# Kernel tuning notes

Hardware: AMD Instinct MI355X
Metric: run time of the kernel (lower is better)

## Reference

```python
import jax, jax.numpy as jnp
import numpy as np

B, F = 4096, 2048          # batch, inp_dim
H, D = 16, 128             # head_num, head_dim
NB, DB = 16, 8             # BlockLinear: head_dim split into head_num blocks of size head_dim//head_num
KER = 4
PROJ = int((4.0 / 3.0) * H * D)   # 2730
LN_EPS = float(F)          # flax quirk: nn.LayerNorm(inp_dim) sets epsilon positionally -> epsilon = 2048.0
GN_EPS = 1e-6              # flax GroupNorm default epsilon
EPS = 1e-8                 # module eps


def setup_inputs() -> dict:
    key = jax.random.key(0)
    ks = jax.random.split(key, 16)
    s = 0.02  # weight init scale for numerical sanity
    hd = H * D
    d = {}
    d['inputs'] = jax.random.normal(ks[0], (B, F), jnp.float32)
    d['c'] = jax.random.normal(ks[1], (B, hd), jnp.float32)
    d['n'] = jnp.ones((B, hd), jnp.float32)
    d['h'] = jax.random.normal(ks[2], (B, hd), jnp.float32)
    d['m'] = jnp.zeros((B, hd), jnp.float32)
    d['x_prev'] = jax.random.normal(ks[3], (B, KER - 1, F), jnp.float32)
    d['ln_scale'] = jnp.ones((F,), jnp.float32)
    d['ln_bias'] = jnp.zeros((F,), jnp.float32)
    for i, g in enumerate('zifo'):
        d['W' + g + '_k'] = jax.random.normal(ks[4 + i], (F, hd), jnp.float32) * s
        d['W' + g + '_b'] = jnp.zeros((hd,), jnp.float32)
        d['R' + g + '_k'] = jax.random.normal(ks[8 + i], (NB, DB, DB), jnp.float32) * s
        d['R' + g + '_b'] = jnp.zeros((NB, DB), jnp.float32)
    d['gn_scale'] = jnp.ones((D,), jnp.float32)
    d['gn_bias'] = jnp.zeros((D,), jnp.float32)
    d['up_k'] = jax.random.normal(ks[12], (hd, 2 * PROJ), jnp.float32) * s
    d['up_b'] = jnp.zeros((2 * PROJ,), jnp.float32)
    d['down_k'] = jax.random.normal(ks[13], (PROJ, F), jnp.float32) * s
    d['down_b'] = jnp.zeros((F,), jnp.float32)
    return d


def _layer_norm(x, scale, bias, eps):
    mu = x.mean(-1, keepdims=True)
    var = x.var(-1, keepdims=True)
    return (x - mu) / jnp.sqrt(var + eps) * scale + bias


def _group_norm(x, scale, bias, eps):
    # x: (B, H, D); flax GroupNorm(num_groups=H) groups the channel (last) dim,
    # reducing over all non-batch axes within each group.
    b, hh, dd = x.shape
    xg = x.reshape(b, hh, H, dd // H)
    mu = xg.mean(axis=(1, 3), keepdims=True)
    var = xg.var(axis=(1, 3), keepdims=True)
    xn = ((xg - mu) / jnp.sqrt(var + eps)).reshape(b, hh, dd)
    return xn * scale + bias


def reference(inputs, c, n, h, m, x_prev, ln_scale, ln_bias,
              Wz_k, Wz_b, Rz_k, Rz_b, Wi_k, Wi_b, Ri_k, Ri_b,
              Wf_k, Wf_b, Rf_k, Rf_b, Wo_k, Wo_b, Ro_k, Ro_b,
              gn_scale, gn_bias, up_k, up_b, down_k, down_b):
    x_t = _layer_norm(inputs, ln_scale, ln_bias, LN_EPS)
    x_window = jnp.concatenate([x_prev, x_t[:, None, :]], axis=1)  # (B, KER, F)
    x_prev_new = x_window[:, 1:, :]
    x_c = x_t  # use_conv == False

    h4 = h.reshape(B, H, NB, DB)  # per-head block-split hidden

    def gate(Wk, Wb, Rk, Rb):
        rec = jnp.einsum('bhnd,nde->bhne', h4, Rk) + Rb  # block-diagonal recurrence
        return x_c @ Wk + Wb + rec.reshape(B, H * D)

    i_raw = gate(Wi_k, Wi_b, Ri_k, Ri_b)
    f_raw = gate(Wf_k, Wf_b, Rf_k, Rf_b)
    z_raw = gate(Wz_k, Wz_b, Rz_k, Rz_b)
    o_raw = gate(Wo_k, Wo_b, Ro_k, Ro_b)

    logfplusm = m + jax.nn.log_sigmoid(f_raw)
    m_t = jnp.where(jnp.all(n == 0.0, axis=-1, keepdims=True), i_raw,
                    jnp.maximum(i_raw, logfplusm))
    o_t = jax.nn.sigmoid(o_raw)
    i_t = jnp.exp(i_raw - m_t)
    f_t = jnp.exp(logfplusm - m_t)
    z_t = jnp.tanh(z_raw)

    c_t = f_t * c + i_t * z_t
    n_t = f_t * n + i_t
    h_t = o_t * (c_t / (n_t + EPS))

    outn = _group_norm(h_t.reshape(B, H, D), gn_scale, gn_bias, GN_EPS).reshape(B, H * D)
    u = outn @ up_k + up_b
    o1, o2 = jnp.split(u, 2, axis=-1)
    out = (o1 * jax.nn.gelu(o2)) @ down_k + down_b + inputs
    return (out, c_t, n_t, h_t, m_t, x_prev_new)
```

## Files before the change

### kernel.cpp

```cpp
#include <hip/hip_runtime.h>
#include <hip/hip_bf16.h>
#include <cstdint>

#define BB 4096
#define FF 2048
#define HD 2048
#define PROJ_N 2730
#define UPN 5460
#define UPN_PAD 5504
#define DK_PAD 2752

typedef __attribute__((ext_vector_type(8))) short bf16x8;
typedef __attribute__((ext_vector_type(4))) float f32x4;

__device__ __forceinline__ unsigned short f2bf(float f) {
  union { float f; unsigned int u; } x; x.f = f;
  unsigned int r = x.u + 0x7fffu + ((x.u >> 16) & 1u);
  return (unsigned short)(r >> 16);
}

__global__ __launch_bounds__(256) void ln_prep(
    const float* __restrict__ inputs, const float* __restrict__ x_prev,
    const float* __restrict__ n_state,
    const float* __restrict__ ln_scale, const float* __restrict__ ln_bias,
    unsigned short* __restrict__ x_t_bf, float* __restrict__ xprev_out,
    int* __restrict__ flags)
{
  int b = blockIdx.x, t = threadIdx.x;
  const float* row = inputs + ((long)b << 11);
  float x[8];
  {
    float4 a = *(const float4*)(row + t * 8);
    float4 c = *(const float4*)(row + t * 8 + 4);
    x[0]=a.x; x[1]=a.y; x[2]=a.z; x[3]=a.w; x[4]=c.x; x[5]=c.y; x[6]=c.z; x[7]=c.w;
  }
  float s = 0.f, sq = 0.f;
#pragma unroll
  for (int k = 0; k < 8; ++k) { s += x[k]; sq += x[k] * x[k]; }

  const float* nrow = n_state + ((long)b << 11);
  int nz;
  {
    float4 a = *(const float4*)(nrow + t * 8);
    float4 c = *(const float4*)(nrow + t * 8 + 4);
    nz = (a.x != 0.f) | (a.y != 0.f) | (a.z != 0.f) | (a.w != 0.f) |
         (c.x != 0.f) | (c.y != 0.f) | (c.z != 0.f) | (c.w != 0.f);
  }

#pragma unroll
  for (int off = 32; off >= 1; off >>= 1) {
    s  += __shfl_xor(s, off);
    sq += __shfl_xor(sq, off);
  }
  __shared__ float ws_s[4], ws_q[4];
  __shared__ int s_nz;
  if (t == 0) s_nz = 0;
  __syncthreads();
  if (nz) s_nz = 1;
  int wave = t >> 6;
  if ((t & 63) == 0) { ws_s[wave] = s; ws_q[wave] = sq; }
  __syncthreads();
  float ts = ws_s[0] + ws_s[1] + ws_s[2] + ws_s[3];
  float tq = ws_q[0] + ws_q[1] + ws_q[2] + ws_q[3];
  float mu  = ts * (1.f / 2048.f);
  float var = tq * (1.f / 2048.f) - mu * mu;
  float rs  = rsqrtf(var + 2048.0f);

  unsigned short outb[8];
  float y[8];
#pragma unroll
  for (int k = 0; k < 8; ++k) {
    int c = t * 8 + k;
    float v = (x[k] - mu) * rs * ln_scale[c] + ln_bias[c];
    y[k] = v;
    outb[k] = f2bf(v);
  }
  *(uint4*)&x_t_bf[((long)b << 11) + t * 8] = *(uint4*)outb;
  float* xo = xprev_out + (long)b * 6144 + 4096 + t * 8;
  *(float4*)(xo)     = make_float4(y[0], y[1], y[2], y[3]);
  *(float4*)(xo + 4) = make_float4(y[4], y[5], y[6], y[7]);
  const float* src = x_prev + (long)b * 6144 + 2048;
  float* dst = xprev_out + (long)b * 6144;
  for (int i = t; i < 1024; i += 256)
    *(float4*)(dst + i * 4) = *(const float4*)(src + i * 4);
  if (t == 0) flags[b] = (s_nz == 0) ? 1 : 0;
}

__global__ __launch_bounds__(256) void transpose_cast(
    const float* __restrict__ in, unsigned short* __restrict__ out,
    int R, int C, int OC, int OK)
{
  __shared__ float tile[32][33];
  int ro0 = blockIdx.x * 32;
  int co0 = blockIdx.y * 32;
  int tx = threadIdx.x & 31, ty = threadIdx.x >> 5;
#pragma unroll
  for (int i = 0; i < 4; ++i) {
    int r = ro0 + ty + i * 8, cc = co0 + tx;
    float v = (r < R && cc < C) ? in[(long)r * C + cc] : 0.f;
    tile[ty + i * 8][tx] = v;
  }
  __syncthreads();
#pragma unroll
  for (int i = 0; i < 4; ++i) {
    int oc = co0 + ty + i * 8, ok = ro0 + tx;
    if (oc < OC && ok < OK)
      out[(long)oc * OK + ok] = f2bf(tile[tx][ty + i * 8]);
  }
}

__global__ __launch_bounds__(256) void gemm_nt(
    const unsigned short* __restrict__ A, const unsigned short* __restrict__ Bt,
    float* __restrict__ C, int K, int lda, int ldb, int ldc,
    const float* __restrict__ bias, const float* __restrict__ resid,
    long strideB, long strideC)
{
  Bt += (long)blockIdx.z * strideB;
  C  += (long)blockIdx.z * strideC;
  __shared__ unsigned short As[128 * 32];
  __shared__ unsigned short Bs[128 * 32];
  int tid = threadIdx.x;
  int lane = tid & 63, wave = tid >> 6;
  int wm = wave >> 1, wn = wave & 1;
  int quad = lane >> 4, m16 = lane & 15;
  int m0 = blockIdx.y * 128, n0 = blockIdx.x * 128;

  int srow = wave * 32 + (lane >> 2);
  int scol = (lane & 3) * 8;
  const unsigned short* ga0 = A  + (long)(m0 + srow) * lda + scol;
  const unsigned short* gb0 = Bt + (long)(n0 + srow) * ldb + scol;
  const unsigned short* ga1 = ga0 + 16L * lda;
  const unsigned short* gb1 = gb0 + 16L * ldb;
  unsigned short* la0 = &As[(wave * 32) * 32];
  unsigned short* la1 = &As[(wave * 32 + 16) * 32];
  unsigned short* lb0 = &Bs[(wave * 32) * 32];
  unsigned short* lb1 = &Bs[(wave * 32 + 16) * 32];

  f32x4 acc[4][4] = {};

  for (int k0 = 0; k0 < K; k0 += 32) {
    __syncthreads();
    __builtin_amdgcn_global_load_lds(
        (const __attribute__((address_space(1))) void*)(ga0 + k0),
        (__attribute__((address_space(3))) void*)la0, 16, 0, 0);
    __builtin_amdgcn_global_load_lds(
        (const __attribute__((address_space(1))) void*)(ga1 + k0),
        (__attribute__((address_space(3))) void*)la1, 16, 0, 0);
    __builtin_amdgcn_global_load_lds(
        (const __attribute__((address_space(1))) void*)(gb0 + k0),
        (__attribute__((address_space(3))) void*)lb0, 16, 0, 0);
    __builtin_amdgcn_global_load_lds(
        (const __attribute__((address_space(1))) void*)(gb1 + k0),
        (__attribute__((address_space(3))) void*)lb1, 16, 0, 0);
    __syncthreads();
    bf16x8 af[4], bfr[4];
#pragma unroll
    for (int i = 0; i < 4; ++i) {
      af[i]  = *(const bf16x8*)&As[(wm * 64 + i * 16 + m16) * 32 + quad * 8];
      bfr[i] = *(const bf16x8*)&Bs[(wn * 64 + i * 16 + m16) * 32 + quad * 8];
    }
#pragma unroll
    for (int i = 0; i < 4; ++i)
#pragma unroll
      for (int j = 0; j < 4; ++j)
        acc[i][j] = __builtin_amdgcn_mfma_f32_16x16x32_bf16(af[i], bfr[j], acc[i][j], 0, 0, 0);
  }

#pragma unroll
  for (int i = 0; i < 4; ++i) {
    int gmb = m0 + wm * 64 + i * 16 + quad * 4;
#pragma unroll
    for (int j = 0; j < 4; ++j) {
      int gn = n0 + wn * 64 + j * 16 + m16;
      float badd = bias ? bias[gn] : 0.f;
#pragma unroll
      for (int r = 0; r < 4; ++r) {
        int gm = gmb + r;
        float v = acc[i][j][r] + badd;
        if (resid) v += resid[(long)gm * ldc + gn];
        C[(long)gm * ldc + gn] = v;
      }
    }
  }
}

__global__ __launch_bounds__(256) void slstm_pointwise(
    const float* __restrict__ g_i, const float* __restrict__ g_f,
    const float* __restrict__ g_z, const float* __restrict__ g_o,
    const float* __restrict__ Wib, const float* __restrict__ Wfb,
    const float* __restrict__ Wzb, const float* __restrict__ Wob,
    const float* __restrict__ Ri, const float* __restrict__ Rf,
    const float* __restrict__ Rz, const float* __restrict__ Ro,
    const float* __restrict__ Rib, const float* __restrict__ Rfb,
    const float* __restrict__ Rzb, const float* __restrict__ Rob,
    const float* __restrict__ c_in, const float* __restrict__ n_in,
    const float* __restrict__ h_in, const float* __restrict__ m_in,
    const int* __restrict__ flags,
    float* __restrict__ c_out, float* __restrict__ n_out,
    float* __restrict__ h_out, float* __restrict__ m_out)
{
  int idx = blockIdx.x * 256 + threadIdx.x;
  int b = idx >> 11, j = idx & 2047;
  int hh = j >> 7, nb = (j >> 3) & 15, e = j & 7;
  const float* hp = h_in + ((long)b << 11) + hh * 128 + nb * 8;
  float hv[8];
#pragma unroll
  for (int d = 0; d < 8; ++d) hv[d] = hp[d];
  int rb = nb * 64 + e;
  float reci = Rib[nb * 8 + e], recf = Rfb[nb * 8 + e];
  float recz = Rzb[nb * 8 + e], reco = Rob[nb * 8 + e];
#pragma unroll
  for (int d = 0; d < 8; ++d) {
    reci += hv[d] * Ri[rb + d * 8];
    recf += hv[d] * Rf[rb + d * 8];
    recz += hv[d] * Rz[rb + d * 8];
    reco += hv[d] * Ro[rb + d * 8];
  }
  float iraw = g_i[idx] + Wib[j] + reci;
  float fraw = g_f[idx] + Wfb[j] + recf;
  float zraw = g_z[idx] + Wzb[j] + recz;
  float oraw = g_o[idx] + Wob[j] + reco;
  float mo = m_in[idx];
  float ls = fminf(fraw, 0.f) - log1pf(expf(-fabsf(fraw)));
  float lfpm = mo + ls;
  float mt = flags[b] ? iraw : fmaxf(iraw, lfpm);
  float ot = 1.f / (1.f + expf(-oraw));
  float it = expf(iraw - mt);
  float ft = expf(lfpm - mt);
  float zt = tanhf(zraw);
  float ct = ft * c_in[idx] + it * zt;
  float nt = ft * n_in[idx] + it;
  float ht = ot * ct / (nt + 1e-8f);
  c_out[idx] = ct; n_out[idx] = nt; h_out[idx] = ht; m_out[idx] = mt;
}

__global__ __launch_bounds__(256) void groupnorm(
    const float* __restrict__ h_t, const float* __restrict__ gn_scale,
    const float* __restrict__ gn_bias, unsigned short* __restrict__ outn)
{
  int b = blockIdx.x, t = threadIdx.x;
  const float* row = h_t + ((long)b << 11);
  float x[8];
  {
    float4 a = *(const float4*)(row + t * 8);
    float4 c = *(const float4*)(row + t * 8 + 4);
    x[0]=a.x; x[1]=a.y; x[2]=a.z; x[3]=a.w; x[4]=c.x; x[5]=c.y; x[6]=c.z; x[7]=c.w;
  }
  float s = 0.f, sq = 0.f;
#pragma unroll
  for (int k = 0; k < 8; ++k) { s += x[k]; sq += x[k] * x[k]; }
  __shared__ float s1[256], s2[256];
  s1[t] = s; s2[t] = sq;
  __syncthreads();
  for (int st = 128; st >= 16; st >>= 1) {
    if (t < st) { s1[t] += s1[t + st]; s2[t] += s2[t + st]; }
    __syncthreads();
  }
  int g = t & 15;
  float mu  = s1[g] * (1.f / 128.f);
  float var = s2[g] * (1.f / 128.f) - mu * mu;
  float rs  = rsqrtf(var + 1e-6f);
  unsigned short ob[8];
#pragma unroll
  for (int k = 0; k < 8; ++k) {
    int j = t * 8 + k;
    int dd = j & 127;
    ob[k] = f2bf((x[k] - mu) * rs * gn_scale[dd] + gn_bias[dd]);
  }
  *(uint4*)&outn[((long)b << 11) + t * 8] = *(uint4*)ob;
}

__global__ __launch_bounds__(256) void gelu_mult(
    const float* __restrict__ u, const float* __restrict__ up_b,
    unsigned short* __restrict__ Hg)
{
  int idx = blockIdx.x * 256 + threadIdx.x;
  if (idx >= BB * DK_PAD) return;
  int b = idx / DK_PAD, p = idx - b * DK_PAD;
  unsigned short r = 0;
  if (p < PROJ_N) {
    const float* ur = u + (long)b * UPN_PAD;
    float o1 = ur[p] + up_b[p];
    float o2 = ur[PROJ_N + p] + up_b[PROJ_N + p];
    float tt = o2 + 0.044715f * o2 * o2 * o2;
    float g = 0.5f * o2 * (1.f + tanhf(0.7978845608028654f * tt));
    r = f2bf(o1 * g);
  }
  Hg[idx] = r;
}

extern "C" void kernel_launch(void* const* d_in, const int* in_sizes, int n_in,
                              void* d_out, int out_size, void* d_ws, size_t ws_size,
                              hipStream_t stream)
{
  const float* inputs  = (const float*)d_in[0];
  const float* c_in    = (const float*)d_in[1];
  const float* n_st    = (const float*)d_in[2];
  const float* h_in    = (const float*)d_in[3];
  const float* m_in    = (const float*)d_in[4];
  const float* x_prev  = (const float*)d_in[5];
  const float* ln_s    = (const float*)d_in[6];
  const float* ln_b    = (const float*)d_in[7];
  const float* Wz = (const float*)d_in[8];  const float* Wzb = (const float*)d_in[9];
  const float* Rz = (const float*)d_in[10]; const float* Rzb = (const float*)d_in[11];
  const float* Wi = (const float*)d_in[12]; const float* Wib = (const float*)d_in[13];
  const float* Ri = (const float*)d_in[14]; const float* Rib = (const float*)d_in[15];
  const float* Wf = (const float*)d_in[16]; const float* Wfb = (const float*)d_in[17];
  const float* Rf = (const float*)d_in[18]; const float* Rfb = (const float*)d_in[19];
  const float* Wo = (const float*)d_in[20]; const float* Wob = (const float*)d_in[21];
  const float* Ro = (const float*)d_in[22]; const float* Rob = (const float*)d_in[23];
  const float* gn_s = (const float*)d_in[24]; const float* gn_b = (const float*)d_in[25];
  const float* up_k = (const float*)d_in[26]; const float* up_b = (const float*)d_in[27];
  const float* dn_k = (const float*)d_in[28]; const float* dn_b = (const float*)d_in[29];

  char* ws = (char*)d_ws;
  float* g_raw = (float*)ws;
  float* u_buf = (float*)ws;
  unsigned short* x_t_bf = (unsigned short*)(ws + 134217728);
  unsigned short* outn_bf = x_t_bf;
  unsigned short* Wt  = (unsigned short*)(ws + 150994944);
  unsigned short* upT = (unsigned short*)(ws + 184549376);
  unsigned short* Hg  = upT;
  unsigned short* dkT = (unsigned short*)(ws + 207093760);
  int* flags = (int*)(ws + 218365952);

  float* out   = (float*)d_out;
  float* out_c = out + (long)1 * 8388608;
  float* out_n = out + (long)2 * 8388608;
  float* out_h = out + (long)3 * 8388608;
  float* out_m = out + (long)4 * 8388608;
  float* out_xp = out + (long)5 * 8388608;

  ln_prep<<<BB, 256, 0, stream>>>(inputs, x_prev, n_st, ln_s, ln_b, x_t_bf, out_xp, flags);

  transpose_cast<<<dim3(64, 64), 256, 0, stream>>>(Wi, Wt + 0L * 4194304, 2048, 2048, 2048, 2048);
  transpose_cast<<<dim3(64, 64), 256, 0, stream>>>(Wf, Wt + 1L * 4194304, 2048, 2048, 2048, 2048);
  transpose_cast<<<dim3(64, 64), 256, 0, stream>>>(Wz, Wt + 2L * 4194304, 2048, 2048, 2048, 2048);
  transpose_cast<<<dim3(64, 64), 256, 0, stream>>>(Wo, Wt + 3L * 4194304, 2048, 2048, 2048, 2048);
  transpose_cast<<<dim3(64, 172), 256, 0, stream>>>(up_k, upT, 2048, UPN, UPN_PAD, 2048);
  transpose_cast<<<dim3(86, 64), 256, 0, stream>>>(dn_k, dkT, PROJ_N, 2048, 2048, DK_PAD);

  gemm_nt<<<dim3(16, 32, 4), 256, 0, stream>>>(x_t_bf, Wt, g_raw,
      2048, 2048, 2048, 2048, nullptr, nullptr, 4194304L, 8388608L);

  slstm_pointwise<<<32768, 256, 0, stream>>>(
      g_raw, g_raw + 8388608L, g_raw + 2L * 8388608, g_raw + 3L * 8388608,
      Wib, Wfb, Wzb, Wob, Ri, Rf, Rz, Ro, Rib, Rfb, Rzb, Rob,
      c_in, n_st, h_in, m_in, flags, out_c, out_n, out_h, out_m);

  groupnorm<<<BB, 256, 0, stream>>>(out_h, gn_s, gn_b, outn_bf);

  gemm_nt<<<dim3(UPN_PAD / 128, 32, 1), 256, 0, stream>>>(outn_bf, upT, u_buf,
      2048, 2048, 2048, UPN_PAD, nullptr, nullptr, 0L, 0L);

  gelu_mult<<<(BB * DK_PAD) / 256, 256, 0, stream>>>(u_buf, up_b, Hg);

  gemm_nt<<<dim3(16, 32, 1), 256, 0, stream>>>(Hg, dkT, out,
      DK_PAD, DK_PAD, DK_PAD, 2048, dn_b, inputs, 0L, 0L);
}
```

Baseline: 1.167 ms.

## Replace bf16 MFMA GEMM with 256x256 double-buffered swizzled LDS pipeline kernel

Replaces the 128x128, 256-thread GEMM with a 512-thread kernel that computes 256x256 output tiles using a K-step of 64. Global-to-LDS loads are double-buffered and interleaved with MFMA phases, which are wrapped in barrier and setprio sequences. LDS uses an XOR swizzle to avoid bank conflicts, and workgroups are remapped across XCDs for cache locality. The intent is to raise MFMA utilisation and data reuse in the three projection GEMMs. The cost is 128 KB of LDS per block, lower occupancy, and padded or clamped tiles on the up-projection, whose N is not a multiple of 256.

```diff
diff --git a/kernel.cpp b/kernel.cpp
--- a/kernel.cpp
+++ b/kernel.cpp
@@ -109,76 +109,153 @@
   }
 }
 
-__global__ __launch_bounds__(256) void gemm_nt(
+#define P_PRE()  do { __builtin_amdgcn_s_barrier(); \
+                      asm volatile("s_waitcnt lgkmcnt(0)" ::: "memory"); \
+                      __builtin_amdgcn_sched_barrier(0); \
+                      __builtin_amdgcn_s_setprio(1); } while (0)
+#define P_POST() do { __builtin_amdgcn_s_setprio(0); \
+                      __builtin_amdgcn_sched_barrier(0); \
+                      __builtin_amdgcn_s_barrier(); \
+                      __builtin_amdgcn_sched_barrier(0); } while (0)
+
+#define STAGE_A(h, k2, bo, kt)                                               \
+  __builtin_amdgcn_global_load_lds(                                          \
+      (const __attribute__((address_space(1))) void*)(pA[h][k2] + (long)(kt)*64), \
+      (__attribute__((address_space(3))) void*)(ldsA + (bo) + ((k2)*16384 + (h)*8192) + wvu*1024), \
+      16, 0, 0)
+#define STAGE_B(cb, i, bo, kt)                                               \
+  __builtin_amdgcn_global_load_lds(                                          \
+      (const __attribute__((address_space(1))) void*)(pB[cb][i] + (long)(kt)*64), \
+      (__attribute__((address_space(3))) void*)(ldsB + (bo) + ((cb)*16384 + (i)*8192) + wvu*1024), \
+      16, 0, 0)
+
+#define LOAD_A(rb, bo)                                                       \
+  { _Pragma("unroll")                                                        \
+    for (int f = 0; f < 4; ++f) {                                            \
+      const char* p_ = ldsA + (bo) + (unsigned)((wm*128 + (rb)*64 + f*16 + m16) << 7); \
+      aF[f][0] = *(const bf16x8*)(p_ + s0);                                  \
+      aF[f][1] = *(const bf16x8*)(p_ + s1);                                  \
+    } }
+#define LOAD_B(cb, BV, bo)                                                   \
+  { _Pragma("unroll")                                                        \
+    for (int f = 0; f < 2; ++f) {                                            \
+      const char* p_ = ldsB + (bo) + (unsigned)(((cb)*128 + wn*32 + f*16 + m16) << 7); \
+      BV[f][0] = *(const bf16x8*)(p_ + s0);                                  \
+      BV[f][1] = *(const bf16x8*)(p_ + s1);                                  \
+    } }
+#define MFMA_PH(rb, cb, BV)                                                  \
+  { _Pragma("unroll")                                                        \
+    for (int f = 0; f < 4; ++f) {                                            \
+      acc[(rb)*4+f][(cb)*2+0] = __builtin_amdgcn_mfma_f32_16x16x32_bf16(     \
+          aF[f][0], BV[0][0], acc[(rb)*4+f][(cb)*2+0], 0, 0, 0);             \
+      acc[(rb)*4+f][(cb)*2+1] = __builtin_amdgcn_mfma_f32_16x16x32_bf16(     \
+          aF[f][0], BV[1][0], acc[(rb)*4+f][(cb)*2+1], 0, 0, 0);             \
+      acc[(rb)*4+f][(cb)*2+0] = __builtin_amdgcn_mfma_f32_16x16x32_bf16(     \
+          aF[f][1], BV[0][1], acc[(rb)*4+f][(cb)*2+0], 0, 0, 0);             \
+      acc[(rb)*4+f][(cb)*2+1] = __builtin_amdgcn_mfma_f32_16x16x32_bf16(     \
+          aF[f][1], BV[1][1], acc[(rb)*4+f][(cb)*2+1], 0, 0, 0);             \
+    } }
+
+__global__ __launch_bounds__(512) void gemm8(
     const unsigned short* __restrict__ A, const unsigned short* __restrict__ Bt,
     float* __restrict__ C, int K, int lda, int ldb, int ldc,
+    int Nreal, int NBmax,
     const float* __restrict__ bias, const float* __restrict__ resid,
     long strideB, long strideC)
 {
+  __shared__ __attribute__((aligned(1024))) char smem[131072];
+  char* ldsA = smem;
+  char* ldsB = smem + 65536;
+
   Bt += (long)blockIdx.z * strideB;
   C  += (long)blockIdx.z * strideC;
-  __shared__ unsigned short As[128 * 32];
-  __shared__ unsigned short Bs[128 * 32];
-  int tid = threadIdx.x;
-  int lane = tid & 63, wave = tid >> 6;
-  int wm = wave >> 1, wn = wave & 1;
-  int quad = lane >> 4, m16 = lane & 15;
-  int m0 = blockIdx.y * 128, n0 = blockIdx.x * 128;
-
-  int srow = wave * 32 + (lane >> 2);
-  int scol = (lane & 3) * 8;
-  const unsigned short* ga0 = A  + (long)(m0 + srow) * lda + scol;
-  const unsigned short* gb0 = Bt + (long)(n0 + srow) * ldb + scol;
-  const unsigned short* ga1 = ga0 + 16L * lda;
-  const unsigned short* gb1 = gb0 + 16L * ldb;
-  unsigned short* la0 = &As[(wave * 32) * 32];
-  unsigned short* la1 = &As[(wave * 32 + 16) * 32];
-  unsigned short* lb0 = &Bs[(wave * 32) * 32];
-  unsigned short* lb1 = &Bs[(wave * 32 + 16) * 32];
-
-  f32x4 acc[4][4] = {};
-
-  for (int k0 = 0; k0 < K; k0 += 32) {
-    __syncthreads();
-    __builtin_amdgcn_global_load_lds(
-        (const __attribute__((address_space(1))) void*)(ga0 + k0),
-        (__attribute__((address_space(3))) void*)la0, 16, 0, 0);
-    __builtin_amdgcn_global_load_lds(
-        (const __attribute__((address_space(1))) void*)(ga1 + k0),
-        (__attribute__((address_space(3))) void*)la1, 16, 0, 0);
-    __builtin_amdgcn_global_load_lds(
-        (const __attribute__((address_space(1))) void*)(gb0 + k0),
-        (__attribute__((address_space(3))) void*)lb0, 16, 0, 0);
-    __builtin_amdgcn_global_load_lds(
-        (const __attribute__((address_space(1))) void*)(gb1 + k0),
-        (__attribute__((address_space(3))) void*)lb1, 16, 0, 0);
-    __syncthreads();
-    bf16x8 af[4], bfr[4];
-#pragma unroll
-    for (int i = 0; i < 4; ++i) {
-      af[i]  = *(const bf16x8*)&As[(wm * 64 + i * 16 + m16) * 32 + quad * 8];
-      bfr[i] = *(const bf16x8*)&Bs[(wn * 64 + i * 16 + m16) * 32 + quad * 8];
+
+  const int tid  = threadIdx.x;
+  const int lane = tid & 63, wvu = tid >> 6;
+  const int wm = wvu >> 2, wn = wvu & 3;
+  const int m16 = lane & 15, qd = lane >> 4;
+
+  int nwg = gridDim.x * gridDim.y;
+  int lin = blockIdx.y * gridDim.x + blockIdx.x;
+  int qq_ = nwg >> 3, rr_ = nwg & 7, xcd = lin & 7, idx8 = lin >> 3;
+  int swz = (xcd < rr_ ? xcd * (qq_ + 1) : rr_ * (qq_ + 1) + (xcd - rr_) * qq_) + idx8;
+  int bx = swz % gridDim.x, by = swz / gridDim.x;
+  const int n0 = bx * 256, m0 = by * 256;
+
+  const int l8 = lane >> 3, l7 = lane & 7;
+  const int scol = ((l7 ^ l8) << 3);
+  const unsigned short *pA[2][2], *pB[2][2];
+#pragma unroll
+  for (int h = 0; h < 2; ++h)
+#pragma unroll
+    for (int k2 = 0; k2 < 2; ++k2) {
+      int row = m0 + k2 * 128 + h * 64 + wvu * 8 + l8;
+      pA[h][k2] = A + (long)row * lda + scol;
     }
 #pragma unroll
-    for (int i = 0; i < 4; ++i)
-#pragma unroll
-      for (int j = 0; j < 4; ++j)
-        acc[i][j] = __builtin_amdgcn_mfma_f32_16x16x32_bf16(af[i], bfr[j], acc[i][j], 0, 0, 0);
-  }
-
-#pragma unroll
-  for (int i = 0; i < 4; ++i) {
-    int gmb = m0 + wm * 64 + i * 16 + quad * 4;
-#pragma unroll
-    for (int j = 0; j < 4; ++j) {
-      int gn = n0 + wn * 64 + j * 16 + m16;
-      float badd = bias ? bias[gn] : 0.f;
-#pragma unroll
-      for (int r = 0; r < 4; ++r) {
-        int gm = gmb + r;
-        float v = acc[i][j][r] + badd;
-        if (resid) v += resid[(long)gm * ldc + gn];
-        C[(long)gm * ldc + gn] = v;
+  for (int cb = 0; cb < 2; ++cb)
+#pragma unroll
+    for (int i = 0; i < 2; ++i) {
+      int qq = i * 64 + wvu * 8 + l8;
+      int n  = ((qq >> 5) << 6) + cb * 32 + (qq & 31);
+      int gr = n0 + n; if (gr > NBmax - 1) gr = NBmax - 1;
+      pB[cb][i] = Bt + (long)gr * ldb + scol;
+    }
+
+  const int s0 = ((qd ^ (m16 & 7)) << 4);
+  const int s1 = s0 ^ 64;
+
+  f32x4 acc[8][4] = {};
+  bf16x8 aF[4][2], b0v[2][2], b1v[2][2];
+
+  const int NT  = K >> 6;
+  const int t1p = (NT > 1) ? 1 : 0;
+
+  STAGE_A(0,0,0,0); STAGE_A(0,1,0,0);
+  STAGE_B(0,0,0,0); STAGE_B(0,1,0,0);
+  STAGE_B(1,0,0,0); STAGE_B(1,1,0,0);
+  STAGE_A(1,0,0,0); STAGE_A(1,1,0,0);
+  STAGE_A(0,0,32768,t1p); STAGE_A(0,1,32768,t1p);
+  STAGE_A(1,0,32768,t1p); STAGE_A(1,1,32768,t1p);
+  asm volatile("s_waitcnt vmcnt(4)" ::: "memory");
+  __builtin_amdgcn_s_barrier();
+  __builtin_amdgcn_sched_barrier(0);
+
+  for (int t = 0; t < NT; ++t) {
+    const int co = (t & 1) << 15;
+    const int oo = co ^ 32768;
+    const int t1 = (t + 1 < NT) ? t + 1 : NT - 1;
+    const int t2 = (t + 2 < NT) ? t + 2 : NT - 1;
+    LOAD_A(0, co);
+    LOAD_B(0, b0v, co);
+    STAGE_B(0,0,oo,t1); STAGE_B(0,1,oo,t1);
+    STAGE_B(1,0,oo,t1); STAGE_B(1,1,oo,t1);
+    P_PRE(); MFMA_PH(0,0,b0v); P_POST();
+    LOAD_B(1, b1v, co);
+    STAGE_A(0,0,co,t2); STAGE_A(0,1,co,t2);
+    P_PRE(); MFMA_PH(0,1,b1v); P_POST();
+    LOAD_A(1, co);
+    P_PRE(); MFMA_PH(1,1,b1v); P_POST();
+    STAGE_A(1,0,co,t2); STAGE_A(1,1,co,t2);
+    asm volatile("s_waitcnt vmcnt(4)" ::: "memory");
+    P_PRE(); MFMA_PH(1,0,b0v); P_POST();
+  }
+  asm volatile("s_waitcnt vmcnt(0)" ::: "memory");
+
+#pragma unroll
+  for (int mf = 0; mf < 8; ++mf) {
+    int gm = m0 + wm * 128 + mf * 16 + qd * 4;
+#pragma unroll
+    for (int nf = 0; nf < 4; ++nf) {
+      int gn = n0 + wn * 64 + nf * 16 + m16;
+      if (gn < Nreal) {
+        float badd = bias ? bias[gn] : 0.f;
+#pragma unroll
+        for (int r = 0; r < 4; ++r) {
+          float v = acc[mf][nf][r] + badd;
+          if (resid) v += resid[(long)(gm + r) * ldc + gn];
+          C[(long)(gm + r) * ldc + gn] = v;
+        }
       }
     }
   }
@@ -340,8 +417,8 @@
   transpose_cast<<<dim3(64, 172), 256, 0, stream>>>(up_k, upT, 2048, UPN, UPN_PAD, 2048);
   transpose_cast<<<dim3(86, 64), 256, 0, stream>>>(dn_k, dkT, PROJ_N, 2048, 2048, DK_PAD);
 
-  gemm_nt<<<dim3(16, 32, 4), 256, 0, stream>>>(x_t_bf, Wt, g_raw,
-      2048, 2048, 2048, 2048, nullptr, nullptr, 4194304L, 8388608L);
+  gemm8<<<dim3(8, 16, 4), 512, 0, stream>>>(x_t_bf, Wt, g_raw,
+      2048, 2048, 2048, 2048, 2048, 2048, nullptr, nullptr, 4194304L, 8388608L);
 
   slstm_pointwise<<<32768, 256, 0, stream>>>(
       g_raw, g_raw + 8388608L, g_raw + 2L * 8388608, g_raw + 3L * 8388608,
@@ -350,11 +427,11 @@
 
   groupnorm<<<BB, 256, 0, stream>>>(out_h, gn_s, gn_b, outn_bf);
 
-  gemm_nt<<<dim3(UPN_PAD / 128, 32, 1), 256, 0, stream>>>(outn_bf, upT, u_buf,
-      2048, 2048, 2048, UPN_PAD, nullptr, nullptr, 0L, 0L);
+  gemm8<<<dim3(22, 16, 1), 512, 0, stream>>>(outn_bf, upT, u_buf,
+      2048, 2048, 2048, UPN_PAD, UPN_PAD, UPN_PAD, nullptr, nullptr, 0L, 0L);
 
   gelu_mult<<<(BB * DK_PAD) / 256, 256, 0, stream>>>(u_buf, up_b, Hg);
 
-  gemm_nt<<<dim3(16, 32, 1), 256, 0, stream>>>(Hg, dkT, out,
-      DK_PAD, DK_PAD, DK_PAD, 2048, dn_b, inputs, 0L, 0L);
-}
+  gemm8<<<dim3(8, 16, 1), 512, 0, stream>>>(Hg, dkT, out,
+      DK_PAD, DK_PAD, DK_PAD, 2048, 2048, 2048, dn_b, inputs, 0L, 0L);
+}
```

Measured after the change: 1.112 ms. 1.05x faster.
